# Performance work log

Measured on AMD Instinct MI355X. Metric: run time of the kernel, lower is better.

## Reference

```python
import jax, jax.numpy as jnp
import numpy as np

HIDDEN = 2048
HEADS = 16
HEAD_DIM = HIDDEN // HEADS


def setup_inputs() -> dict:
    key = jax.random.key(0)
    ks = jax.random.split(key, 9)
    s = 1.0 / np.sqrt(HIDDEN)
    return {
        "hidden_states": jax.random.normal(ks[0], (2, 2048, HIDDEN), dtype=jnp.float32),
        "wq": jax.random.uniform(ks[1], (HIDDEN, HIDDEN), jnp.float32, -s, s),
        "bq": jax.random.uniform(ks[2], (HIDDEN,), jnp.float32, -s, s),
        "wk": jax.random.uniform(ks[3], (HIDDEN, HIDDEN), jnp.float32, -s, s),
        "bk": jax.random.uniform(ks[4], (HIDDEN,), jnp.float32, -s, s),
        "wv": jax.random.uniform(ks[5], (HIDDEN, HIDDEN), jnp.float32, -s, s),
        "bv": jax.random.uniform(ks[6], (HIDDEN,), jnp.float32, -s, s),
        "wo": jax.random.uniform(ks[7], (HIDDEN, HIDDEN), jnp.float32, -s, s),
        "bo": jax.random.uniform(ks[8], (HIDDEN,), jnp.float32, -s, s),
    }


def reference(hidden_states, wq, bq, wk, bk, wv, bv, wo, bo):
    B, S, _ = hidden_states.shape
    # QKV projections (nn.Linear: x @ W^T + b)
    q = hidden_states @ wq.T + bq
    k = hidden_states @ wk.T + bk
    v = hidden_states @ wv.T + bv
    # [B, S, H, D] -> [B, H, S, D]
    q = q.reshape(B, S, HEADS, HEAD_DIM).transpose(0, 2, 1, 3)
    k = k.reshape(B, S, HEADS, HEAD_DIM).transpose(0, 2, 1, 3)
    v = v.reshape(B, S, HEADS, HEAD_DIM).transpose(0, 2, 1, 3)
    scale = HEAD_DIM ** (-0.5)
    scores = jnp.einsum("bhqd,bhkd->bhqk", q, k) * scale  # [B,H,S,S]
    attn = jax.nn.softmax(scores, axis=-1)
    out = jnp.einsum("bhqk,bhkd->bhqd", attn, v)
    out = out.transpose(0, 2, 1, 3).reshape(B, S, HIDDEN)
    return out @ wo.T + bo
```

## Files before the change

### kernel.cpp

```cpp
#include <hip/hip_runtime.h>
#include <math.h>

#define HID 2048
#define NB  2
#define SEQ 2048
#define NT  (NB*SEQ)
#define NH  16
#define HD  128

typedef __attribute__((ext_vector_type(8))) _Float16       f16x8;
typedef __attribute__((ext_vector_type(4))) float          f32x4;

#define QSCALE 0.12751742f

__device__ __forceinline__ unsigned short f2h(float x) {
    union { _Float16 h; unsigned short u; } c;
    c.h = (_Float16)x;
    return c.u;
}

extern "C" __global__ __launch_bounds__(256)
void cast_all(const float* __restrict__ X,
              const float* __restrict__ w0, const float* __restrict__ w1,
              const float* __restrict__ w2, const float* __restrict__ w3,
              unsigned short* __restrict__ Xd,
              unsigned short* __restrict__ d0, unsigned short* __restrict__ d1,
              unsigned short* __restrict__ d2, unsigned short* __restrict__ d3,
              int n4x, int n4w)
{
    const int y = blockIdx.y;
    const float* __restrict__ src =
        (y==0) ? X : (y==1) ? w0 : (y==2) ? w1 : (y==3) ? w2 : w3;
    unsigned short* __restrict__ dst =
        (y==0) ? Xd : (y==1) ? d0 : (y==2) ? d1 : (y==3) ? d2 : d3;
    const int n4 = (y==0) ? n4x : n4w;
    const int i = blockIdx.x * 256 + threadIdx.x;
    if (i >= n4) return;
    const float4 x = ((const float4*)src)[i];
    ushort4 h;
    h.x = f2h(x.x); h.y = f2h(x.y); h.z = f2h(x.z); h.w = f2h(x.w);
    ((ushort4*)dst)[i] = h;
}

extern "C" __global__ __launch_bounds__(256)
void qkv_f16(const unsigned short* __restrict__ Xh,
             const unsigned short* __restrict__ Wqh,
             const unsigned short* __restrict__ Wkh,
             const unsigned short* __restrict__ Wvh,
             const float* __restrict__ bq, const float* __restrict__ bk,
             const float* __restrict__ bv,
             unsigned short* __restrict__ Qb, unsigned short* __restrict__ Kb,
             unsigned short* __restrict__ Vb)
{
    const int on0 = blockIdx.x * 128;
    const int tm0 = blockIdx.y * 128;
    const int which = blockIdx.z;
    const unsigned short* __restrict__ W = (which==0) ? Wqh : (which==1) ? Wkh : Wvh;
    const float* __restrict__ bias      = (which==0) ? bq  : (which==1) ? bk  : bv;

    __shared__ unsigned short Ah[8192], Bh[8192];

    const int tid  = threadIdx.x;
    const int lane = tid & 63;
    const int w    = tid >> 6;
    const int wm   = (w & 1) * 64;
    const int wn   = (w >> 1) * 64;
    const int fr   = lane & 15;
    const int quad = lane >> 4;

    f32x4 acc[4][4];
    #pragma unroll
    for (int i = 0; i < 4; ++i)
        #pragma unroll
        for (int j = 0; j < 4; ++j)
            acc[i][j] = (f32x4){0.f, 0.f, 0.f, 0.f};

    for (int kb = 0; kb < HID/64; ++kb) {
        __syncthreads();
        const unsigned short* Asrc = Xh + (size_t)tm0*HID + kb*64;
        const unsigned short* Bsrc = W  + (size_t)on0*HID + kb*64;
        #pragma unroll
        for (int r = 0; r < 4; ++r) {
            const int p   = (r*4 + w)*64 + lane;
            const int row = p >> 3;
            const int c   = (p & 7) ^ (row & 7);
            __builtin_amdgcn_global_load_lds(
                (const __attribute__((address_space(1))) void*)(Asrc + (size_t)row*HID + c*8),
                (__attribute__((address_space(3))) void*)(Ah + (r*4 + w)*512), 16, 0, 0);
            __builtin_amdgcn_global_load_lds(
                (const __attribute__((address_space(1))) void*)(Bsrc + (size_t)row*HID + c*8),
                (__attribute__((address_space(3))) void*)(Bh + (r*4 + w)*512), 16, 0, 0);
        }
        __syncthreads();

        #pragma unroll
        for (int kk = 0; kk < 2; ++kk) {
            f16x8 a[4], b[4];
            #pragma unroll
            for (int i = 0; i < 4; ++i) {
                const int ra = wm + i*16 + fr;
                a[i] = *(const f16x8*)(Ah + (ra*8 + ((kk*4 + quad) ^ (ra & 7)))*8);
                const int rb = wn + i*16 + fr;
                b[i] = *(const f16x8*)(Bh + (rb*8 + ((kk*4 + quad) ^ (rb & 7)))*8);
            }
            #pragma unroll
            for (int i = 0; i < 4; ++i)
                #pragma unroll
                for (int j = 0; j < 4; ++j)
                    acc[i][j] = __builtin_amdgcn_mfma_f32_16x16x32_f16(a[i], b[j], acc[i][j], 0, 0, 0);
        }
    }

    const int col_l = fr;
    if (which == 2) {
        #pragma unroll
        for (int j = 0; j < 4; ++j) {
            const int o = on0 + wn + j*16 + col_l;
            const float bb = bias[o];
            const int h = o >> 7, d = o & (HD-1);
            #pragma unroll
            for (int i = 0; i < 4; ++i)
                #pragma unroll
                for (int rg = 0; rg < 4; ++rg) {
                    const int t = tm0 + wm + i*16 + quad*4 + rg;
                    const int b = t >> 11, s = t & (SEQ-1);
                    Vb[((size_t)(b*NH + h)*HD + d)*SEQ + s] = f2h(acc[i][j][rg] + bb);
                }
        }
    } else {
        const float sc = (which == 0) ? QSCALE : 1.0f;
        unsigned short* __restrict__ dstp = (which == 0) ? Qb : Kb;
        #pragma unroll
        for (int j = 0; j < 4; ++j) {
            const int o = on0 + wn + j*16 + col_l;
            const float bb = bias[o];
            const int h = o >> 7, d = o & (HD-1);
            #pragma unroll
            for (int i = 0; i < 4; ++i)
                #pragma unroll
                for (int rg = 0; rg < 4; ++rg) {
                    const int t = tm0 + wm + i*16 + quad*4 + rg;
                    const int b = t >> 11, s = t & (SEQ-1);
                    dstp[((size_t)(b*NH + h)*SEQ + s)*HD + d] =
                        f2h((acc[i][j][rg] + bb) * sc);
                }
        }
    }
}

extern "C" __global__ __launch_bounds__(512, 4)
void attn_mfma(const unsigned short* __restrict__ Qg, const unsigned short* __restrict__ Kg,
               const unsigned short* __restrict__ Vtg, unsigned short* __restrict__ Of)
{
    const int L  = blockIdx.x;
    const int q0 = (L >> 5) * 128;
    const int bh = ((L & 7) << 2) | ((L >> 3) & 3);
    const unsigned short* __restrict__ Qp = Qg  + (size_t)bh * SEQ * HD;
    const unsigned short* __restrict__ Kp = Kg  + (size_t)bh * SEQ * HD;
    const unsigned short* __restrict__ Vp = Vtg + (size_t)bh * HD * SEQ;

    __shared__ alignas(16) unsigned short Ks[2][64*128];
    __shared__ alignas(16) unsigned short Vts[2][128*64];
    __shared__ alignas(16) unsigned short Ps[128*64];

    const int tid  = threadIdx.x;
    const int lane = tid & 63;
    const int w    = tid >> 6;
    const int iq   = w >> 1;
    const int js   = w & 1;
    const int fr   = lane & 15;
    const int quad = lane >> 4;

    f16x8 qf[2][4];
    #pragma unroll
    for (int m = 0; m < 2; ++m)
        #pragma unroll
        for (int c = 0; c < 4; ++c)
            qf[m][c] = *(const f16x8*)(Qp + (size_t)(q0 + iq*32 + m*16 + fr)*HD
                                          + c*32 + quad*8);

    f32x4 accO[2][4];
    #pragma unroll
    for (int m = 0; m < 2; ++m)
        #pragma unroll
        for (int n = 0; n < 4; ++n)
            accO[m][n] = (f32x4){0.f, 0.f, 0.f, 0.f};
    float lp[2][4] = {};

#define STAGE(buf, kt_) do {                                                   \
    const unsigned short* _Kt = Kp + (size_t)(kt_)*64*HD;                      \
    _Pragma("unroll")                                                          \
    for (int _r = 0; _r < 2; ++_r) {                                           \
        const int _p = (_r*8 + w)*64 + lane;                                   \
        const int _row = _p >> 4;                                              \
        const int _c = (_p & 15) ^ (_row & 15);                                \
        __builtin_amdgcn_global_load_lds(                                      \
            (const __attribute__((address_space(1))) void*)(_Kt + (size_t)_row*HD + _c*8), \
            (__attribute__((address_space(3))) void*)(&Ks[buf][_p*8]), 16, 0, 0); \
    }                                                                          \
    _Pragma("unroll")                                                          \
    for (int _r = 0; _r < 2; ++_r) {                                           \
        const int _p = (_r*8 + w)*64 + lane;                                   \
        const int _row = _p >> 3;                                              \
        const int _c = (_p & 7) ^ (_row & 7);                                  \
        __builtin_amdgcn_global_load_lds(                                      \
            (const __attribute__((address_space(1))) void*)(Vp + (size_t)_row*SEQ + (kt_)*64 + _c*8), \
            (__attribute__((address_space(3))) void*)(&Vts[buf][_p*8]), 16, 0, 0); \
    } } while (0)

    STAGE(0, 0);
    __syncthreads();

    int cur = 0;
    for (int kt = 0; kt < SEQ/64; ++kt) {
        if (kt + 1 < SEQ/64) STAGE(cur ^ 1, kt + 1);

        const unsigned short* Kc = &Ks[cur][0];
        const unsigned short* Vc = &Vts[cur][0];

        f32x4 accS[2][2];
        #pragma unroll
        for (int m = 0; m < 2; ++m)
            #pragma unroll
            for (int n = 0; n < 2; ++n)
                accS[m][n] = (f32x4){0.f, 0.f, 0.f, 0.f};
        #pragma unroll
        for (int c = 0; c < 4; ++c) {
            f16x8 bf[2];
            #pragma unroll
            for (int n = 0; n < 2; ++n)
                bf[n] = *(const f16x8*)(Kc + (js*32 + n*16 + fr)*128
                                           + (((c*4 + quad) ^ fr) << 3));
            __builtin_amdgcn_s_setprio(1);
            #pragma unroll
            for (int m = 0; m < 2; ++m)
                #pragma unroll
                for (int n = 0; n < 2; ++n)
                    accS[m][n] = __builtin_amdgcn_mfma_f32_16x16x32_f16(
                        qf[m][c], bf[n], accS[m][n], 0, 0, 0);
            __builtin_amdgcn_s_setprio(0);
        }

        #pragma unroll
        for (int m = 0; m < 2; ++m)
            #pragma unroll
            for (int n = 0; n < 2; ++n)
                #pragma unroll
                for (int rg = 0; rg < 4; ++rg) {
                    const float p = exp2f(accS[m][n][rg]);
                    lp[m][rg] += p;
                    const int q = iq*32 + m*16 + quad*4 + rg;
                    const int s = js*32 + n*16 + fr;
                    Ps[q*64 + ((((s >> 3) ^ (q & 7)) << 3) | (s & 7))] = f2h(p);
                }
        asm volatile("s_waitcnt lgkmcnt(0)" ::: "memory");
        __builtin_amdgcn_s_barrier();
        __builtin_amdgcn_sched_barrier(0);

        #pragma unroll
        for (int kk = 0; kk < 2; ++kk) {
            f16x8 pf[2], vf[4];
            #pragma unroll
            for (int m = 0; m < 2; ++m)
                pf[m] = *(const f16x8*)(Ps + (iq*32 + m*16 + fr)*64
                                           + (((kk*4 + quad) ^ (fr & 7)) << 3));
            #pragma unroll
            for (int n = 0; n < 4; ++n)
                vf[n] = *(const f16x8*)(Vc + (js*64 + n*16 + fr)*64
                                           + (((kk*4 + quad) ^ (fr & 7)) << 3));
            __builtin_amdgcn_s_setprio(1);
            #pragma unroll
            for (int m = 0; m < 2; ++m)
                #pragma unroll
                for (int n = 0; n < 4; ++n)
                    accO[m][n] = __builtin_amdgcn_mfma_f32_16x16x32_f16(
                        pf[m], vf[n], accO[m][n], 0, 0, 0);
            __builtin_amdgcn_s_setprio(0);
        }

        asm volatile("s_waitcnt vmcnt(0) lgkmcnt(0)" ::: "memory");
        __builtin_amdgcn_s_barrier();
        __builtin_amdgcn_sched_barrier(0);
        cur ^= 1;
    }
#undef STAGE

    float lred[2][4];
    #pragma unroll
    for (int m = 0; m < 2; ++m)
        #pragma unroll
        for (int rg = 0; rg < 4; ++rg) {
            float l = lp[m][rg];
            l += __shfl_xor(l, 1);
            l += __shfl_xor(l, 2);
            l += __shfl_xor(l, 4);
            l += __shfl_xor(l, 8);
            lred[m][rg] = l;
        }
    float* Ls = (float*)(&Ks[0][0]);
    if (fr == 0) {
        #pragma unroll
        for (int m = 0; m < 2; ++m)
            #pragma unroll
            for (int rg = 0; rg < 4; ++rg)
                Ls[w*32 + m*16 + quad*4 + rg] = lred[m][rg];
    }
    __syncthreads();

    const int bb_ = bh >> 4;
    const int hh_ = bh & (NH - 1);
    #pragma unroll
    for (int m = 0; m < 2; ++m) {
        float inv[4];
        #pragma unroll
        for (int rg = 0; rg < 4; ++rg)
            inv[rg] = 1.0f / (lred[m][rg] + Ls[(w ^ 1)*32 + m*16 + quad*4 + rg]);
        #pragma unroll
        for (int n = 0; n < 4; ++n) {
            const int d = js*64 + n*16 + fr;
            #pragma unroll
            for (int rg = 0; rg < 4; ++rg) {
                const int s = q0 + iq*32 + m*16 + quad*4 + rg;
                Of[((size_t)(bb_*SEQ + s))*HID + hh_*HD + d] = f2h(accO[m][n][rg] * inv[rg]);
            }
        }
    }
}

extern "C" __global__ __launch_bounds__(256)
void oproj_f16(const unsigned short* __restrict__ Af,
               const unsigned short* __restrict__ Woh,
               const float* __restrict__ bo, float* __restrict__ Y)
{
    const int on0 = blockIdx.x * 128;
    const int tm0 = blockIdx.y * 64;

    __shared__ unsigned short Ah[4096], Bh[8192];

    const int tid  = threadIdx.x;
    const int lane = tid & 63;
    const int w    = tid >> 6;
    const int wm   = (w & 1) * 32;
    const int wn   = (w >> 1) * 64;
    const int fr   = lane & 15;
    const int quad = lane >> 4;

    f32x4 acc[2][4];
    #pragma unroll
    for (int i = 0; i < 2; ++i)
        #pragma unroll
        for (int j = 0; j < 4; ++j)
            acc[i][j] = (f32x4){0.f, 0.f, 0.f, 0.f};

    for (int kb = 0; kb < HID/64; ++kb) {
        __syncthreads();
        const unsigned short* Asrc = Af  + (size_t)tm0*HID + kb*64;
        const unsigned short* Bsrc = Woh + (size_t)on0*HID + kb*64;
        #pragma unroll
        for (int r = 0; r < 2; ++r) {
            const int p   = r*256 + tid;
            const int row = p >> 3;
            const int c   = (p & 7) ^ (row & 7);
            __builtin_amdgcn_global_load_lds(
                (const __attribute__((address_space(1))) void*)(Asrc + (size_t)row*HID + c*8),
                (__attribute__((address_space(3))) void*)(Ah + p*8), 16, 0, 0);
        }
        #pragma unroll
        for (int r = 0; r < 4; ++r) {
            const int p   = r*256 + tid;
            const int row = p >> 3;
            const int c   = (p & 7) ^ (row & 7);
            __builtin_amdgcn_global_load_lds(
                (const __attribute__((address_space(1))) void*)(Bsrc + (size_t)row*HID + c*8),
                (__attribute__((address_space(3))) void*)(Bh + p*8), 16, 0, 0);
        }
        __syncthreads();

        #pragma unroll
        for (int kk = 0; kk < 2; ++kk) {
            f16x8 a[2], b[4];
            #pragma unroll
            for (int i = 0; i < 2; ++i) {
                const int ra = wm + i*16 + fr;
                a[i] = *(const f16x8*)(Ah + (ra*8 + ((kk*4 + quad) ^ (ra & 7)))*8);
            }
            #pragma unroll
            for (int j = 0; j < 4; ++j) {
                const int rb = wn + j*16 + fr;
                b[j] = *(const f16x8*)(Bh + (rb*8 + ((kk*4 + quad) ^ (rb & 7)))*8);
            }
            #pragma unroll
            for (int i = 0; i < 2; ++i)
                #pragma unroll
                for (int j = 0; j < 4; ++j)
                    acc[i][j] = __builtin_amdgcn_mfma_f32_16x16x32_f16(a[i], b[j], acc[i][j], 0, 0, 0);
        }
    }

    #pragma unroll
    for (int j = 0; j < 4; ++j) {
        const int o = on0 + wn + j*16 + fr;
        const float bb = bo[o];
        #pragma unroll
        for (int i = 0; i < 2; ++i)
            #pragma unroll
            for (int rg = 0; rg < 4; ++rg) {
                const int t = tm0 + wm + i*16 + quad*4 + rg;
                Y[(size_t)t*HID + o] = acc[i][j][rg] + bb;
            }
    }
}

extern "C" void kernel_launch(void* const* d_in, const int* in_sizes, int n_in,
                              void* d_out, int out_size, void* d_ws, size_t ws_size,
                              hipStream_t stream)
{
    const float* X  = (const float*)d_in[0];
    const float* wq = (const float*)d_in[1];
    const float* bq = (const float*)d_in[2];
    const float* wk = (const float*)d_in[3];
    const float* bk = (const float*)d_in[4];
    const float* wv = (const float*)d_in[5];
    const float* bv = (const float*)d_in[6];
    const float* wo = (const float*)d_in[7];
    const float* bo = (const float*)d_in[8];
    float* Y = (float*)d_out;

    const size_t F  = (size_t)NT * HID;
    const size_t Wn = (size_t)HID * HID;

    unsigned short* Qb  = (unsigned short*)d_ws;
    unsigned short* Kb  = Qb  + F;
    unsigned short* Vb  = Kb  + F;
    unsigned short* Of  = Vb  + F;
    unsigned short* Xh  = Of  + F;
    unsigned short* Wqh = Xh  + F;
    unsigned short* Wkh = Wqh + Wn;
    unsigned short* Wvh = Wkh + Wn;
    unsigned short* Woh = Wvh + Wn;

    const int n4x = (int)(F/4);
    const int n4w = (int)(Wn/4);

    cast_all<<<dim3((n4x + 255)/256, 5), 256, 0, stream>>>(
        X, wq, wk, wv, wo, Xh, Wqh, Wkh, Wvh, Woh, n4x, n4w);

    qkv_f16<<<dim3(HID/128, NT/128, 3), 256, 0, stream>>>(
        Xh, Wqh, Wkh, Wvh, bq, bk, bv, Qb, Kb, Vb);

    attn_mfma<<<dim3(512, 1, 1), 512, 0, stream>>>(Qb, Kb, Vb, Of);

    oproj_f16<<<dim3(HID/128, NT/64), 256, 0, stream>>>(Of, Woh, bo, Y);
}
```

Measured before the change: 452.6 us.

## Permute V sequence layout to pack P stores and drop K/V double buffering

The V projection epilogue now writes the sequence index through a permutation so that each lane's two softmax probabilities can be packed into one 32-bit store into a padded P tile, using a packed round-toward-zero convert. This replaces the scalar XOR-swizzled P stores. The K/V double-buffered async staging is replaced by a single buffer loaded at the top of each iteration between two barriers, which shrinks shared memory to raise occupancy but no longer overlaps global loads with compute. The LDS destination addressing for the async loads also changes to per-wave bases.

```diff
diff --git a/kernel.cpp b/kernel.cpp
--- a/kernel.cpp
+++ b/kernel.cpp
@@ -9,6 +9,7 @@
 #define HD  128
 
 typedef __attribute__((ext_vector_type(8))) _Float16       f16x8;
+typedef __attribute__((ext_vector_type(2))) __fp16         h16x2;
 typedef __attribute__((ext_vector_type(4))) float          f32x4;
 
 #define QSCALE 0.12751742f
@@ -17,6 +18,10 @@
     union { _Float16 h; unsigned short u; } c;
     c.h = (_Float16)x;
     return c.u;
+}
+
+__device__ __forceinline__ int sigmap(int s) {
+    return (s & ~63) | (((s & 15) << 2) | (((s >> 5) & 1) << 1) | ((s >> 4) & 1));
 }
 
 extern "C" __global__ __launch_bounds__(256)
@@ -124,7 +129,8 @@
                 for (int rg = 0; rg < 4; ++rg) {
                     const int t = tm0 + wm + i*16 + quad*4 + rg;
                     const int b = t >> 11, s = t & (SEQ-1);
-                    Vb[((size_t)(b*NH + h)*HD + d)*SEQ + s] = f2h(acc[i][j][rg] + bb);
+                    const int pos = sigmap(s);
+                    Vb[((size_t)(b*NH + h)*HD + d)*SEQ + pos] = f2h(acc[i][j][rg] + bb);
                 }
         }
     } else {
@@ -147,6 +153,8 @@
         }
     }
 }
+
+#define PS_STRIDE 72
 
 extern "C" __global__ __launch_bounds__(512, 4)
 void attn_mfma(const unsigned short* __restrict__ Qg, const unsigned short* __restrict__ Kg,
@@ -159,9 +167,9 @@
     const unsigned short* __restrict__ Kp = Kg  + (size_t)bh * SEQ * HD;
     const unsigned short* __restrict__ Vp = Vtg + (size_t)bh * HD * SEQ;
 
-    __shared__ alignas(16) unsigned short Ks[2][64*128];
-    __shared__ alignas(16) unsigned short Vts[2][128*64];
-    __shared__ alignas(16) unsigned short Ps[128*64];
+    __shared__ alignas(16) unsigned short Ks[64*128];
+    __shared__ alignas(16) unsigned short Vts[128*64];
+    __shared__ alignas(16) unsigned short Ps[128*PS_STRIDE];
 
     const int tid  = threadIdx.x;
     const int lane = tid & 63;
@@ -187,36 +195,30 @@
             accO[m][n] = (f32x4){0.f, 0.f, 0.f, 0.f};
     float lp[2][4] = {};
 
-#define STAGE(buf, kt_) do {                                                   \
-    const unsigned short* _Kt = Kp + (size_t)(kt_)*64*HD;                      \
-    _Pragma("unroll")                                                          \
-    for (int _r = 0; _r < 2; ++_r) {                                           \
-        const int _p = (_r*8 + w)*64 + lane;                                   \
-        const int _row = _p >> 4;                                              \
-        const int _c = (_p & 15) ^ (_row & 15);                                \
-        __builtin_amdgcn_global_load_lds(                                      \
-            (const __attribute__((address_space(1))) void*)(_Kt + (size_t)_row*HD + _c*8), \
-            (__attribute__((address_space(3))) void*)(&Ks[buf][_p*8]), 16, 0, 0); \
-    }                                                                          \
-    _Pragma("unroll")                                                          \
-    for (int _r = 0; _r < 2; ++_r) {                                           \
-        const int _p = (_r*8 + w)*64 + lane;                                   \
-        const int _row = _p >> 3;                                              \
-        const int _c = (_p & 7) ^ (_row & 7);                                  \
-        __builtin_amdgcn_global_load_lds(                                      \
-            (const __attribute__((address_space(1))) void*)(Vp + (size_t)_row*SEQ + (kt_)*64 + _c*8), \
-            (__attribute__((address_space(3))) void*)(&Vts[buf][_p*8]), 16, 0, 0); \
-    } } while (0)
-
-    STAGE(0, 0);
-    __syncthreads();
-
-    int cur = 0;
     for (int kt = 0; kt < SEQ/64; ++kt) {
-        if (kt + 1 < SEQ/64) STAGE(cur ^ 1, kt + 1);
-
-        const unsigned short* Kc = &Ks[cur][0];
-        const unsigned short* Vc = &Vts[cur][0];
+        __syncthreads();
+        {
+            const unsigned short* Kt = Kp + (size_t)kt*64*HD;
+            #pragma unroll
+            for (int r = 0; r < 2; ++r) {
+                const int p   = (r*8 + w)*64 + lane;
+                const int row = p >> 4;
+                const int c   = (p & 15) ^ (row & 15);
+                __builtin_amdgcn_global_load_lds(
+                    (const __attribute__((address_space(1))) void*)(Kt + (size_t)row*HD + c*8),
+                    (__attribute__((address_space(3))) void*)(Ks + (r*8 + w)*512), 16, 0, 0);
+            }
+            #pragma unroll
+            for (int r = 0; r < 2; ++r) {
+                const int p   = (r*8 + w)*64 + lane;
+                const int row = p >> 3;
+                const int c   = (p & 7) ^ (row & 7);
+                __builtin_amdgcn_global_load_lds(
+                    (const __attribute__((address_space(1))) void*)(Vp + (size_t)row*SEQ + kt*64 + c*8),
+                    (__attribute__((address_space(3))) void*)(Vts + (r*8 + w)*512), 16, 0, 0);
+            }
+        }
+        __syncthreads();
 
         f32x4 accS[2][2];
         #pragma unroll
@@ -228,9 +230,10 @@
         for (int c = 0; c < 4; ++c) {
             f16x8 bf[2];
             #pragma unroll
-            for (int n = 0; n < 2; ++n)
-                bf[n] = *(const f16x8*)(Kc + (js*32 + n*16 + fr)*128
-                                           + (((c*4 + quad) ^ fr) << 3));
+            for (int n = 0; n < 2; ++n) {
+                const int row = js*32 + n*16 + fr;
+                bf[n] = *(const f16x8*)(Ks + row*128 + (((c*4 + quad) ^ fr) << 3));
+            }
             __builtin_amdgcn_s_setprio(1);
             #pragma unroll
             for (int m = 0; m < 2; ++m)
@@ -244,30 +247,29 @@
         #pragma unroll
         for (int m = 0; m < 2; ++m)
             #pragma unroll
-            for (int n = 0; n < 2; ++n)
-                #pragma unroll
-                for (int rg = 0; rg < 4; ++rg) {
-                    const float p = exp2f(accS[m][n][rg]);
-                    lp[m][rg] += p;
-                    const int q = iq*32 + m*16 + quad*4 + rg;
-                    const int s = js*32 + n*16 + fr;
-                    Ps[q*64 + ((((s >> 3) ^ (q & 7)) << 3) | (s & 7))] = f2h(p);
-                }
-        asm volatile("s_waitcnt lgkmcnt(0)" ::: "memory");
-        __builtin_amdgcn_s_barrier();
-        __builtin_amdgcn_sched_barrier(0);
+            for (int rg = 0; rg < 4; ++rg) {
+                const float p0 = exp2f(accS[m][0][rg]);
+                const float p1 = exp2f(accS[m][1][rg]);
+                lp[m][rg] += p0 + p1;
+                union { h16x2 h; unsigned int u; } pk;
+                pk.h = __builtin_amdgcn_cvt_pkrtz(p0, p1);
+                const int qq = iq*32 + m*16 + quad*4 + rg;
+                *(unsigned int*)(&Ps[qq*PS_STRIDE + fr*4 + js*2]) = pk.u;
+            }
+        __syncthreads();
 
         #pragma unroll
         for (int kk = 0; kk < 2; ++kk) {
             f16x8 pf[2], vf[4];
             #pragma unroll
             for (int m = 0; m < 2; ++m)
-                pf[m] = *(const f16x8*)(Ps + (iq*32 + m*16 + fr)*64
-                                           + (((kk*4 + quad) ^ (fr & 7)) << 3));
-            #pragma unroll
-            for (int n = 0; n < 4; ++n)
-                vf[n] = *(const f16x8*)(Vc + (js*64 + n*16 + fr)*64
-                                           + (((kk*4 + quad) ^ (fr & 7)) << 3));
+                pf[m] = *(const f16x8*)(Ps + (iq*32 + m*16 + fr)*PS_STRIDE
+                                           + kk*32 + quad*8);
+            #pragma unroll
+            for (int n = 0; n < 4; ++n) {
+                const int row = js*64 + n*16 + fr;
+                vf[n] = *(const f16x8*)(Vts + row*64 + (((kk*4 + quad) ^ (fr & 7)) << 3));
+            }
             __builtin_amdgcn_s_setprio(1);
             #pragma unroll
             for (int m = 0; m < 2; ++m)
@@ -277,13 +279,7 @@
                         pf[m], vf[n], accO[m][n], 0, 0, 0);
             __builtin_amdgcn_s_setprio(0);
         }
-
-        asm volatile("s_waitcnt vmcnt(0) lgkmcnt(0)" ::: "memory");
-        __builtin_amdgcn_s_barrier();
-        __builtin_amdgcn_sched_barrier(0);
-        cur ^= 1;
-    }
-#undef STAGE
+    }
 
     float lred[2][4];
     #pragma unroll
@@ -297,7 +293,8 @@
             l += __shfl_xor(l, 8);
             lred[m][rg] = l;
         }
-    float* Ls = (float*)(&Ks[0][0]);
+    __syncthreads();
+    float* Ls = (float*)(&Ks[0]);
     if (fr == 0) {
         #pragma unroll
         for (int m = 0; m < 2; ++m)
```

New measurement: 426.3 us. -5.8%, faster.
